# Kernel optimization log

Hardware: AMD Instinct MI355X
Metric: run time of the kernel (lower is better)

The kernel has to match this reference:

```python
import jax, jax.numpy as jnp
import numpy as np
from jax import lax

# Balloon-Windkessel BOLD hemodynamic model, explicit Euler, 1000 steps.
# getEulerBOLD(mtt, kappa=1.0, gamma=1.0, stim_on=True, n_steps=1000)
# States: s (vasodilatory signal), f (inflow), v (blood volume), q (deoxyhemoglobin).
# BOLD readout: y = V0*(k1*(1-q) + k2*(1 - q/v) + k3*(1 - v))

N_STEPS = 1000
DT = 0.01           # Euler step (s)
ALPHA = 0.32        # Grubb's exponent
RHO = 0.34          # resting oxygen extraction fraction
V0 = 0.02           # resting blood volume fraction
K1 = 7.0 * RHO
K2 = 2.0
K3 = 2.0 * RHO - 0.2
KAPPA = 1.0         # signal decay (2nd arg in source)
GAMMA = 1.0         # flow-dependent elimination (3rd arg in source)


def _euler_bold(mtt):
    u = jnp.ones((N_STEPS,), dtype=mtt.dtype)  # stimulus on (True flag)
    inv_alpha = 1.0 / ALPHA

    def step(carry, u_t):
        s, f, v, q = carry
        v_pow = v ** inv_alpha                       # outflow f_out(v) = v^(1/alpha)
        E = 1.0 - (1.0 - RHO) ** (1.0 / f)           # oxygen extraction E(f)
        ds = u_t - KAPPA * s - GAMMA * (f - 1.0)
        df = s
        dv = (f - v_pow) / mtt
        dq = (f * E / RHO - v_pow * q / v) / mtt
        s = s + DT * ds
        f = f + DT * df
        v = v + DT * dv
        q = q + DT * dq
        y = V0 * (K1 * (1.0 - q) + K2 * (1.0 - q / v) + K3 * (1.0 - v))
        return (s, f, v, q), y

    one = jnp.asarray(1.0, dtype=mtt.dtype)
    zero = jnp.asarray(0.0, dtype=mtt.dtype)
    init = (zero, one, one, one)
    _, ys = lax.scan(step, init, u)
    return ys  # [N_STEPS]


def setup_inputs() -> dict:
    mtt = jnp.asarray(1.0, dtype=jnp.float32)  # nn.Parameter(torch.tensor(1.0))
    return {"mtt": mtt}


def reference(mtt) -> jnp.ndarray:
    return _euler_bold(mtt)
```

## Files before the change

kernel.cpp:

```cpp
#include <hip/hip_runtime.h>
#include <math.h>


namespace {
constexpr int   kChunks = 250;
constexpr float kDt     = 0.01f;
constexpr float kInvRho = 1.0f / 0.34f;
constexpr float kV0 = 0.02f, kK1 = 2.38f, kK2 = 2.0f, kK3 = 0.48f;
constexpr float kLog2R    = -0.0071769251f;
constexpr float kThetaRev =  0.0013852133f;
constexpr float kCB       = -0.57735026919f;
constexpr float kL2OneMR  = -0.5994620704f;
constexpr float kPwm1     = 2.125f;
}

template<int Ctrl, int RowMask>
__device__ __forceinline__ float dppf(float x, float ident) {
    return __int_as_float(__builtin_amdgcn_update_dpp(
        __float_as_int(ident), __float_as_int(x), Ctrl, RowMask, 0xF, false));
}

__device__ __forceinline__ void wave_scan2(float& xP, float& xQ) {
    #define ST(C, M) { float yP = dppf<C, M>(xP, 1.0f);            \
                       float yQ = dppf<C, M>(xQ, 0.0f);            \
                       xQ = fmaf(xP, yQ, xQ); xP *= yP; }
    ST(0x111, 0xF) ST(0x112, 0xF) ST(0x114, 0xF) ST(0x118, 0xF)
    ST(0x142, 0xA) ST(0x143, 0xC)
    #undef ST
}
__device__ __forceinline__ void wave_scan4(float& xP, float& xQ,
                                           float& uP, float& uQ) {
    #define ST(C, M) { float yP = dppf<C, M>(xP, 1.0f);            \
                       float yQ = dppf<C, M>(xQ, 0.0f);            \
                       float zP = dppf<C, M>(uP, 1.0f);            \
                       float zQ = dppf<C, M>(uQ, 0.0f);            \
                       xQ = fmaf(xP, yQ, xQ); xP *= yP;            \
                       uQ = fmaf(uP, zQ, uQ); uP *= zP; }
    ST(0x111, 0xF) ST(0x112, 0xF) ST(0x114, 0xF) ST(0x118, 0xF)
    ST(0x142, 0xA) ST(0x143, 0xC)
    #undef ST
}

__global__ __launch_bounds__(256)
void bold_kernel(const void* __restrict__ mtt_raw, float* __restrict__ out) {
    __shared__ float2 SCv[4];
    __shared__ float2 SCq[4];
    __shared__ float  SCX[4];
    const int tid  = threadIdx.x;
    const int lane = tid & 63, wid = tid >> 6;

    unsigned bits = *(const unsigned*)mtt_raw;
    float mtt = ((bits & 0xFFFFu) == 0u) ? __uint_as_float(bits)
                                         : __uint_as_float(bits << 16);
    const float c1  = kDt / mtt;
    const float c31 = 3.125f * c1;
    const float c21 = kPwm1 * c1;

    float Fc[4] = {0, 0, 0, 0}, Bq[4] = {0, 0, 0, 0};
    if (tid < kChunks) {
        #pragma unroll
        for (int k = 0; k < 4; ++k) {
            float tf = (float)(4 * tid + k);
            float rt = __builtin_amdgcn_exp2f(tf * kLog2R);
            float ar = tf * kThetaRev;
            float sn = __builtin_amdgcn_sinf(ar);
            float cs = __builtin_amdgcn_cosf(ar);
            float ft = fmaf(rt, fmaf(kCB, sn, -cs), 2.0f);
            float E1 = __builtin_amdgcn_exp2f(kL2OneMR * __builtin_amdgcn_rcpf(ft));
            Fc[k] = c1 * ft;
            Bq[k] = (c1 * kInvRho) * ft * (1.0f - E1);
        }
    }

    float4 X = make_float4(1.f, 1.f, 1.f, 1.f);
    float A[4] = {1, 1, 1, 1}, B[4] = {0, 0, 0, 0};

    {
        float Pc = 1.0f, Qc = 0.0f;
        const float A0 = 1.0f - c31;
        if (tid < kChunks) {
            #pragma unroll
            for (int k = 0; k < 4; ++k) {
                A[k] = A0; B[k] = Fc[k] + c21;
                Qc = fmaf(A0, Qc, B[k]); Pc *= A0;
            }
        }
        float xP = Pc, xQ = Qc;
        wave_scan2(xP, xQ);
        if (lane == 63) SCv[wid] = make_float2(xP, xQ);
        __syncthreads();
        float eP = __shfl_up(xP, 1, 64), eQ = __shfl_up(xQ, 1, 64);
        if (lane == 0) { eP = 1.f; eQ = 0.f; }
        float2 a0 = SCv[0], a1 = SCv[1], a2 = SCv[2];
        float wP = 1.f, wQ = 0.f;
        if (wid >= 1) { wP = a0.x; wQ = a0.y; }
        if (wid >= 2) { wQ = fmaf(a1.x, wQ, a1.y); wP *= a1.x; }
        if (wid >= 3) { wQ = fmaf(a2.x, wQ, a2.y); wP *= a2.x; }
        float x = fmaf(eP, wQ, eQ) + eP * wP;
        x = fmaf(A[0], x, B[0]); X.x = x;
        x = fmaf(A[1], x, B[1]); X.y = x;
        x = fmaf(A[2], x, B[2]); X.z = x;
        x = fmaf(A[3], x, B[3]); X.w = x;
        if (lane == 63) SCX[wid] = X.w;
        __syncthreads();
    }

    for (int sw = 0; sw < 3; ++sw) {
        float predw = __shfl_up(X.w, 1, 64);
        float oldw  = (wid == 0) ? 1.0f : SCX[wid - 1];
        if (lane == 0) predw = oldw;
        float Pc = 1.0f, Qc = 0.0f;
        if (tid < kChunks) {
            float vb[4] = {predw, X.x, X.y, X.z};
            #pragma unroll
            for (int k = 0; k < 4; ++k) {
                float w  = __builtin_amdgcn_exp2f(
                               kPwm1 * __builtin_amdgcn_logf(vb[k]));
                float p3 = w * vb[k];
                float At = fmaf(-c31, w, 1.0f);
                float Bt = fmaf(c21, p3, Fc[k]);
                A[k] = At; B[k] = Bt;
                Qc = fmaf(At, Qc, Bt); Pc = At * Pc;
            }
        }
        float xP = Pc, xQ = Qc;
        wave_scan2(xP, xQ);
        if (lane == 63) SCv[wid] = make_float2(xP, xQ);
        __syncthreads();
        float eP = __shfl_up(xP, 1, 64), eQ = __shfl_up(xQ, 1, 64);
        if (lane == 0) { eP = 1.f; eQ = 0.f; }
        float2 a0 = SCv[0], a1 = SCv[1], a2 = SCv[2];
        float wP = 1.f, wQ = 0.f;
        if (wid >= 1) { wP = a0.x; wQ = a0.y; }
        if (wid >= 2) { wQ = fmaf(a1.x, wQ, a1.y); wP *= a1.x; }
        if (wid >= 3) { wQ = fmaf(a2.x, wQ, a2.y); wP *= a2.x; }
        float x = fmaf(eP, wQ, eQ) + eP * wP;
        x = fmaf(A[0], x, B[0]); X.x = x;
        x = fmaf(A[1], x, B[1]); X.y = x;
        x = fmaf(A[2], x, B[2]); X.z = x;
        x = fmaf(A[3], x, B[3]); X.w = x;
        if (lane == 63) SCX[wid] = X.w;
        __syncthreads();
    }

    {
        float predw = __shfl_up(X.w, 1, 64);
        float oldw  = (wid == 0) ? 1.0f : SCX[wid - 1];
        if (lane == 0) predw = oldw;
        float Pv = 1.f, Qv = 0.f, Pq = 1.f, Qq = 0.f;
        float Aq[4] = {1, 1, 1, 1};
        if (tid < kChunks) {
            float vb[4] = {predw, X.x, X.y, X.z};
            #pragma unroll
            for (int k = 0; k < 4; ++k) {
                float w   = __builtin_amdgcn_exp2f(
                                kPwm1 * __builtin_amdgcn_logf(vb[k]));
                float p3  = w * vb[k];
                float At  = fmaf(-c31, w, 1.0f);
                float Bt  = fmaf(c21, p3, Fc[k]);
                float Aqt = fmaf(-c1, w, 1.0f);
                A[k] = At; B[k] = Bt; Aq[k] = Aqt;
                Qv = fmaf(At, Qv, Bt);     Pv = At * Pv;
                Qq = fmaf(Aqt, Qq, Bq[k]); Pq = Aqt * Pq;
            }
        }
        float xP = Pv, xQ = Qv, uP = Pq, uQ = Qq;
        wave_scan4(xP, xQ, uP, uQ);
        if (lane == 63) { SCv[wid] = make_float2(xP, xQ);
                          SCq[wid] = make_float2(uP, uQ); }
        __syncthreads();
        float eP = __shfl_up(xP, 1, 64), eQ = __shfl_up(xQ, 1, 64);
        float fP = __shfl_up(uP, 1, 64), fQ = __shfl_up(uQ, 1, 64);
        if (lane == 0) { eP = 1.f; eQ = 0.f; fP = 1.f; fQ = 0.f; }
        float2 a0 = SCv[0], a1 = SCv[1], a2 = SCv[2];
        float2 b0 = SCq[0], b1 = SCq[1], b2 = SCq[2];
        float wP = 1.f, wQ = 0.f, vP = 1.f, vQ = 0.f;
        if (wid >= 1) { wP = a0.x; wQ = a0.y; vP = b0.x; vQ = b0.y; }
        if (wid >= 2) { wQ = fmaf(a1.x, wQ, a1.y); wP *= a1.x;
                        vQ = fmaf(b1.x, vQ, b1.y); vP *= b1.x; }
        if (wid >= 3) { wQ = fmaf(a2.x, wQ, a2.y); wP *= a2.x;
                        vQ = fmaf(b2.x, vQ, b2.y); vP *= b2.x; }
        if (tid < kChunks) {
            float x = fmaf(eP, wQ, eQ) + eP * wP;
            float q = fmaf(fP, vQ, fQ) + fP * vP;
            float yv[4];
            #pragma unroll
            for (int k = 0; k < 4; ++k) {
                x = fmaf(A[k],  x, B[k]);
                q = fmaf(Aq[k], q, Bq[k]);
                yv[k] = kV0 * (kK1 * (1.0f - q)
                             + kK2 * fmaf(-q, __builtin_amdgcn_rcpf(x), 1.0f)
                             + kK3 * (1.0f - x));
            }
            ((float4*)out)[tid] = make_float4(yv[0], yv[1], yv[2], yv[3]);
        }
    }
}

extern "C" void kernel_launch(void* const* d_in, const int* in_sizes, int n_in,
                              void* d_out, int out_size, void* d_ws, size_t ws_size,
                              hipStream_t stream) {
    bold_kernel<<<dim3(1), dim3(256), 0, stream>>>(d_in[0], (float*)d_out);
}
```

Measured before the change: 53.50 us.

## Drop per-sweep barrier, double-buffer scan carries, use DPP shift, cut one sweep

Each chunk now keeps its own starting state (`xprev`) from the cross-chunk scan instead of fetching the previous chunk's end value through a shuffle plus shared memory. That removes the second `__syncthreads` and the `SCX` buffer in every sweep. The wave carry array is double-buffered so the next sweep's writes cannot race with the current reads. The wave-level shuffle-up is replaced with a DPP wave shift-right. The number of fixed-point refinement sweeps drops from three to two, which shortens the serial dependency chain but may lower accuracy of the volume iterate.

```diff
diff --git a/kernel.cpp b/kernel.cpp
--- a/kernel.cpp
+++ b/kernel.cpp
@@ -43,9 +43,8 @@
 
 __global__ __launch_bounds__(256)
 void bold_kernel(const void* __restrict__ mtt_raw, float* __restrict__ out) {
-    __shared__ float2 SCv[4];
+    __shared__ float2 SCv[2][4];
     __shared__ float2 SCq[4];
-    __shared__ float  SCX[4];
     const int tid  = threadIdx.x;
     const int lane = tid & 63, wid = tid >> 6;
 
@@ -73,6 +72,7 @@
     }
 
     float4 X = make_float4(1.f, 1.f, 1.f, 1.f);
+    float xprev = 1.0f;
     float A[4] = {1, 1, 1, 1}, B[4] = {0, 0, 0, 0};
 
     {
@@ -87,31 +87,29 @@
         }
         float xP = Pc, xQ = Qc;
         wave_scan2(xP, xQ);
-        if (lane == 63) SCv[wid] = make_float2(xP, xQ);
+        if (lane == 63) SCv[0][wid] = make_float2(xP, xQ);
         __syncthreads();
-        float eP = __shfl_up(xP, 1, 64), eQ = __shfl_up(xQ, 1, 64);
-        if (lane == 0) { eP = 1.f; eQ = 0.f; }
-        float2 a0 = SCv[0], a1 = SCv[1], a2 = SCv[2];
+        float eP = dppf<0x138, 0xF>(xP, 1.0f);
+        float eQ = dppf<0x138, 0xF>(xQ, 0.0f);
+        float2 a0 = SCv[0][0], a1 = SCv[0][1], a2 = SCv[0][2];
         float wP = 1.f, wQ = 0.f;
         if (wid >= 1) { wP = a0.x; wQ = a0.y; }
         if (wid >= 2) { wQ = fmaf(a1.x, wQ, a1.y); wP *= a1.x; }
         if (wid >= 3) { wQ = fmaf(a2.x, wQ, a2.y); wP *= a2.x; }
         float x = fmaf(eP, wQ, eQ) + eP * wP;
+        xprev = x;
         x = fmaf(A[0], x, B[0]); X.x = x;
         x = fmaf(A[1], x, B[1]); X.y = x;
         x = fmaf(A[2], x, B[2]); X.z = x;
         x = fmaf(A[3], x, B[3]); X.w = x;
-        if (lane == 63) SCX[wid] = X.w;
-        __syncthreads();
     }
 
-    for (int sw = 0; sw < 3; ++sw) {
-        float predw = __shfl_up(X.w, 1, 64);
-        float oldw  = (wid == 0) ? 1.0f : SCX[wid - 1];
-        if (lane == 0) predw = oldw;
+    #pragma unroll
+    for (int sw = 0; sw < 2; ++sw) {
+        const int buf = 1 - sw;
         float Pc = 1.0f, Qc = 0.0f;
         if (tid < kChunks) {
-            float vb[4] = {predw, X.x, X.y, X.z};
+            float vb[4] = {xprev, X.x, X.y, X.z};
             #pragma unroll
             for (int k = 0; k < 4; ++k) {
                 float w  = __builtin_amdgcn_exp2f(
@@ -125,32 +123,28 @@
         }
         float xP = Pc, xQ = Qc;
         wave_scan2(xP, xQ);
-        if (lane == 63) SCv[wid] = make_float2(xP, xQ);
+        if (lane == 63) SCv[buf][wid] = make_float2(xP, xQ);
         __syncthreads();
-        float eP = __shfl_up(xP, 1, 64), eQ = __shfl_up(xQ, 1, 64);
-        if (lane == 0) { eP = 1.f; eQ = 0.f; }
-        float2 a0 = SCv[0], a1 = SCv[1], a2 = SCv[2];
+        float eP = dppf<0x138, 0xF>(xP, 1.0f);
+        float eQ = dppf<0x138, 0xF>(xQ, 0.0f);
+        float2 a0 = SCv[buf][0], a1 = SCv[buf][1], a2 = SCv[buf][2];
         float wP = 1.f, wQ = 0.f;
         if (wid >= 1) { wP = a0.x; wQ = a0.y; }
         if (wid >= 2) { wQ = fmaf(a1.x, wQ, a1.y); wP *= a1.x; }
         if (wid >= 3) { wQ = fmaf(a2.x, wQ, a2.y); wP *= a2.x; }
         float x = fmaf(eP, wQ, eQ) + eP * wP;
+        xprev = x;
         x = fmaf(A[0], x, B[0]); X.x = x;
         x = fmaf(A[1], x, B[1]); X.y = x;
         x = fmaf(A[2], x, B[2]); X.z = x;
         x = fmaf(A[3], x, B[3]); X.w = x;
-        if (lane == 63) SCX[wid] = X.w;
-        __syncthreads();
     }
 
     {
-        float predw = __shfl_up(X.w, 1, 64);
-        float oldw  = (wid == 0) ? 1.0f : SCX[wid - 1];
-        if (lane == 0) predw = oldw;
         float Pv = 1.f, Qv = 0.f, Pq = 1.f, Qq = 0.f;
         float Aq[4] = {1, 1, 1, 1};
         if (tid < kChunks) {
-            float vb[4] = {predw, X.x, X.y, X.z};
+            float vb[4] = {xprev, X.x, X.y, X.z};
             #pragma unroll
             for (int k = 0; k < 4; ++k) {
                 float w   = __builtin_amdgcn_exp2f(
@@ -166,14 +160,15 @@
         }
         float xP = Pv, xQ = Qv, uP = Pq, uQ = Qq;
         wave_scan4(xP, xQ, uP, uQ);
-        if (lane == 63) { SCv[wid] = make_float2(xP, xQ);
-                          SCq[wid] = make_float2(uP, uQ); }
+        if (lane == 63) { SCv[1][wid] = make_float2(xP, xQ);
+                          SCq[wid]    = make_float2(uP, uQ); }
         __syncthreads();
-        float eP = __shfl_up(xP, 1, 64), eQ = __shfl_up(xQ, 1, 64);
-        float fP = __shfl_up(uP, 1, 64), fQ = __shfl_up(uQ, 1, 64);
-        if (lane == 0) { eP = 1.f; eQ = 0.f; fP = 1.f; fQ = 0.f; }
-        float2 a0 = SCv[0], a1 = SCv[1], a2 = SCv[2];
-        float2 b0 = SCq[0], b1 = SCq[1], b2 = SCq[2];
+        float eP = dppf<0x138, 0xF>(xP, 1.0f);
+        float eQ = dppf<0x138, 0xF>(xQ, 0.0f);
+        float fP = dppf<0x138, 0xF>(uP, 1.0f);
+        float fQ = dppf<0x138, 0xF>(uQ, 0.0f);
+        float2 a0 = SCv[1][0], a1 = SCv[1][1], a2 = SCv[1][2];
+        float2 b0 = SCq[0],    b1 = SCq[1],    b2 = SCq[2];
         float wP = 1.f, wQ = 0.f, vP = 1.f, vQ = 0.f;
         if (wid >= 1) { wP = a0.x; wQ = a0.y; vP = b0.x; vQ = b0.y; }
         if (wid >= 2) { wQ = fmaf(a1.x, wQ, a1.y); wP *= a1.x;
```

Result: no change. 53.83 us (+0.6%).
